# Kernel tuning notes

Hardware: AMD Instinct MI355X
Metric: run time of the kernel (lower is better)

The kernel has to match this reference:

```python
import jax, jax.numpy as jnp
import numpy as np

B, S, D, H = 8, 2048, 1024, 64

def setup_inputs() -> dict:
    key = jax.random.key(0)
    ks = jax.random.split(key, 7)
    scale = 0.02
    return {
        "x": jax.random.normal(ks[0], (B, S, D), dtype=jnp.float32),
        "Wq": jax.random.normal(ks[1], (D, H), dtype=jnp.float32) * scale,
        "bq": jax.random.normal(ks[2], (H,), dtype=jnp.float32) * scale,
        "Wk": jax.random.normal(ks[3], (D, H), dtype=jnp.float32) * scale,
        "bk": jax.random.normal(ks[4], (H,), dtype=jnp.float32) * scale,
        "Wv": jax.random.normal(ks[5], (D, H), dtype=jnp.float32) * scale,
        "bv": jax.random.normal(ks[6], (H,), dtype=jnp.float32) * scale,
    }

def reference(x, Wq, bq, Wk, bk, Wv, bv):
    # Single-head causal self-attention (dropout in eval mode -> identity).
    q = x @ Wq + bq            # [B,S,H]
    k = x @ Wk + bk            # [B,S,H]
    v = x @ Wv + bv            # [B,S,H]
    scores = jnp.einsum("bqh,bkh->bqk", q, k)  # [B,S,S]
    s = q.shape[1]
    causal = jnp.tril(jnp.ones((s, s), dtype=bool))
    # Original masks with -inf BEFORE scaling; -inf/scale == -inf, so equivalent.
    scores = jnp.where(causal, scores, -jnp.inf) / jnp.sqrt(jnp.float32(k.shape[-1]))
    attn = jax.nn.softmax(scores, axis=-1)
    return jnp.einsum("bqk,bkh->bqh", attn, v)
```

## Files before the change

kernel.cpp:

```cpp
#include <hip/hip_runtime.h>
#include <math.h>

#define BATCH 8
#define SEQ   2048
#define DIM   1024
#define HD    64
#define NROWS (BATCH * SEQ)
#define CHUNK 256
#define NCHUNK 8
#define QTILE 32
#define NQT   (SEQ / QTILE)

typedef __attribute__((ext_vector_type(8))) short bf16x8;
typedef __attribute__((ext_vector_type(4))) float f32x4;

__device__ __forceinline__ unsigned short f2bf(float f) {
    unsigned u = __float_as_uint(f);
    u = (u + 0x7FFFu + ((u >> 16) & 1u)) >> 16;
    return (unsigned short)u;
}

__device__ __forceinline__ void gld_lds16(const void* g, void* l) {
    __builtin_amdgcn_global_load_lds(
        (const __attribute__((address_space(1))) void*)g,
        (__attribute__((address_space(3))) void*)l, 16, 0, 0);
}


__global__ __launch_bounds__(256)
void prep_w_kernel(const float* __restrict__ Wq, const float* __restrict__ Wk,
                   const float* __restrict__ Wv, unsigned short* __restrict__ Wt)
{
    const int mat = blockIdx.y;
    const float* __restrict__ W = (mat == 0) ? Wq : (mat == 1) ? Wk : Wv;
    const int k0 = blockIdx.x * 64;
    __shared__ float T[64][65];
    const int t = threadIdx.x;
    #pragma unroll
    for (int i = 0; i < 16; ++i) {
        const int idx = t + i * 256;
        T[idx >> 6][idx & 63] = W[(size_t)(k0 + (idx >> 6)) * HD + (idx & 63)];
    }
    __syncthreads();
    const int n = t >> 2;
    const int c = t & 3;
    union { unsigned short h[16]; uint4 v[2]; } buf;
    #pragma unroll
    for (int j = 0; j < 16; ++j) buf.h[j] = f2bf(T[c * 16 + j][n]);
    unsigned short* dst = Wt + ((size_t)mat * HD + n) * DIM + k0 + c * 16;
    *(uint4*)dst       = buf.v[0];
    *(uint4*)(dst + 8) = buf.v[1];
}

__global__ __launch_bounds__(384)
void qkv_mfma_kernel(const float* __restrict__ x,
                     const unsigned short* __restrict__ Wt,
                     const float* __restrict__ bq, const float* __restrict__ bk,
                     const float* __restrict__ bv,
                     unsigned short* __restrict__ Qg,
                     unsigned short* __restrict__ Kg,
                     unsigned short* __restrict__ Vtg)
{
    __shared__ unsigned short Xs[32][64];
    __shared__ unsigned short Ws[192][64];

    const int t    = threadIdx.x;
    const int lane = t & 63;
    const int w    = t >> 6;
    const int col  = lane & 15;
    const int quad = lane >> 4;
    const int rh   = w & 1;
    const int mat  = w >> 1;
    const int row0 = blockIdx.x * 32;

    const int r8 = lane >> 3, ch = lane & 7;
    const int xr = t >> 3,  xc = t & 7;

    f32x4 acc[4];
    #pragma unroll
    for (int i = 0; i < 4; ++i) acc[i] = (f32x4){0.f, 0.f, 0.f, 0.f};

    const int swzr = (ch ^ r8) * 8;

    for (int k0 = 0; k0 < DIM; k0 += 64) {
        __syncthreads();
        #pragma unroll
        for (int ii = 0; ii < 4; ++ii) {
            const int rbase = w * 32 + ii * 8;
            gld_lds16(&Wt[(size_t)(rbase + r8) * DIM + k0 + swzr], &Ws[rbase][0]);
        }
        if (t < 256) {
            const float* xp = &x[(size_t)(row0 + xr) * DIM + k0 + xc * 8];
            const float4 v0 = *(const float4*)xp;
            const float4 v1 = *(const float4*)(xp + 4);
            uint4 o;
            o.x = (unsigned)f2bf(v0.x) | ((unsigned)f2bf(v0.y) << 16);
            o.y = (unsigned)f2bf(v0.z) | ((unsigned)f2bf(v0.w) << 16);
            o.z = (unsigned)f2bf(v1.x) | ((unsigned)f2bf(v1.y) << 16);
            o.w = (unsigned)f2bf(v1.z) | ((unsigned)f2bf(v1.w) << 16);
            *(uint4*)&Xs[xr][(xc ^ (xr & 7)) * 8] = o;
        }
        __syncthreads();
        #pragma unroll
        for (int ks = 0; ks < 2; ++ks) {
            const int fswz = ((ks * 4 + quad) ^ (col & 7)) * 8;
            const bf16x8 a = *(const bf16x8*)&Xs[rh * 16 + col][fswz];
            #pragma unroll
            for (int nt = 0; nt < 4; ++nt) {
                const bf16x8 b = *(const bf16x8*)&Ws[mat * 64 + nt * 16 + col][fswz];
                acc[nt] = __builtin_amdgcn_mfma_f32_16x16x32_bf16(a, b, acc[nt], 0, 0, 0);
            }
        }
    }

    const int b    = row0 / SEQ;
    const int s0   = (row0 % SEQ) + rh * 16 + quad * 4;
    const int grow = row0 + rh * 16 + quad * 4;
    const float* __restrict__ bias = (mat == 0) ? bq : (mat == 1) ? bk : bv;
    #pragma unroll
    for (int nt = 0; nt < 4; ++nt) {
        const int nn = nt * 16 + col;
        const float bvv = bias[nn];
        if (mat < 2) {
            unsigned short* __restrict__ o = (mat == 0) ? Qg : Kg;
            #pragma unroll
            for (int r = 0; r < 4; ++r)
                o[(size_t)(grow + r) * HD + nn] = f2bf(acc[nt][r] + bvv);
        } else {
            const unsigned lo = (unsigned)f2bf(acc[nt][0] + bvv) | ((unsigned)f2bf(acc[nt][1] + bvv) << 16);
            const unsigned hi = (unsigned)f2bf(acc[nt][2] + bvv) | ((unsigned)f2bf(acc[nt][3] + bvv) << 16);
            *(uint2*)&Vtg[((size_t)b * HD + nn) * SEQ + s0] = make_uint2(lo, hi);
        }
    }
}

__global__ __launch_bounds__(128)
void attn_part_kernel(const unsigned short* __restrict__ Qg,
                      const unsigned short* __restrict__ Kg,
                      const unsigned short* __restrict__ Vtg,
                      float* __restrict__ Opart,
                      float* __restrict__ ML)
{
    const int xb = blockIdx.x;
    const int c  = xb >> 9;
    const int b  = (xb >> 6) & 7;
    const int qt = xb & 63;
    if (qt < c * 8) return;

    __shared__ unsigned short Ks[64][64];
    __shared__ unsigned short Vs[64][64];
    __shared__ unsigned short Ps[2][16][72];

    const int t    = threadIdx.x;
    const int w    = t >> 6;
    const int lane = t & 63;
    const int col  = lane & 15;
    const int quad = lane >> 4;
    const int q0w  = qt * QTILE + w * 16;
    const size_t gq = (size_t)b * SEQ + q0w;

    const bf16x8 aq0 = *(const bf16x8*)&Qg[(gq + col) * HD + quad * 8];
    const bf16x8 aq1 = *(const bf16x8*)&Qg[(gq + col) * HD + 32 + quad * 8];

    f32x4 oacc[4];
    #pragma unroll
    for (int n = 0; n < 4; ++n) oacc[n] = (f32x4){0.f, 0.f, 0.f, 0.f};
    float mrow[4], lrow[4];
    #pragma unroll
    for (int r = 0; r < 4; ++r) { mrow[r] = -INFINITY; lrow[r] = 0.f; }

    const int kbeg   = c * CHUNK;
    const int kend   = min((c + 1) * CHUNK, (qt + 1) * QTILE);
    const int ntiles = (kend - kbeg + 63) >> 6;

    const int r8 = lane >> 3, ch = lane & 7;
    const int swzr = (ch ^ r8) * 8;
    const unsigned short* kgb = Kg  + (size_t)b * SEQ * HD;
    const unsigned short* vgb = Vtg + (size_t)b * HD * SEQ;

    for (int it = 0; it < ntiles; ++it) {
        const int j0 = kbeg + it * 64;
        __syncthreads();
        #pragma unroll
        for (int ii = 0; ii < 4; ++ii) {
            const int rb = w * 32 + ii * 8;
            gld_lds16(&kgb[(size_t)(j0 + rb + r8) * HD + swzr], &Ks[rb][0]);
            gld_lds16(&vgb[(size_t)(rb + r8) * SEQ + j0 + swzr], &Vs[rb][0]);
        }
        __syncthreads();

        if (j0 <= q0w + 15) {
            f32x4 scv[4];
            #pragma unroll
            for (int nt = 0; nt < 4; ++nt) {
                const int sw0 = (quad ^ (col & 7)) * 8;
                const int sw1 = ((4 + quad) ^ (col & 7)) * 8;
                const bf16x8 bk0 = *(const bf16x8*)&Ks[nt * 16 + col][sw0];
                const bf16x8 bk1 = *(const bf16x8*)&Ks[nt * 16 + col][sw1];
                f32x4 s = __builtin_amdgcn_mfma_f32_16x16x32_bf16(aq0, bk0, (f32x4){0.f,0.f,0.f,0.f}, 0, 0, 0);
                s = __builtin_amdgcn_mfma_f32_16x16x32_bf16(aq1, bk1, s, 0, 0, 0);
                scv[nt] = s;
            }
            const bool needmask = (j0 + 63 > q0w);
            #pragma unroll
            for (int r = 0; r < 4; ++r) {
                const int row = q0w + quad * 4 + r;
                float sv[4];
                float tmax = -INFINITY;
                if (needmask) {
                    #pragma unroll
                    for (int nt = 0; nt < 4; ++nt) {
                        const int key = j0 + nt * 16 + col;
                        sv[nt] = (key <= row) ? scv[nt][r] * 0.125f : -INFINITY;
                        tmax = fmaxf(tmax, sv[nt]);
                    }
                } else {
                    #pragma unroll
                    for (int nt = 0; nt < 4; ++nt) {
                        sv[nt] = scv[nt][r] * 0.125f;
                        tmax = fmaxf(tmax, sv[nt]);
                    }
                }
                #pragma unroll
                for (int off = 1; off < 16; off <<= 1)
                    tmax = fmaxf(tmax, __shfl_xor(tmax, off, 64));
                const float mnew  = fmaxf(mrow[r], tmax);
                const float alpha = __expf(mrow[r] - mnew);
                mrow[r] = mnew;
                float psum = 0.f;
                #pragma unroll
                for (int nt = 0; nt < 4; ++nt) {
                    const float p = __expf(sv[nt] - mnew);
                    psum += p;
                    Ps[w][quad * 4 + r][nt * 16 + col] = f2bf(p);
                }
                #pragma unroll
                for (int off = 1; off < 16; off <<= 1)
                    psum += __shfl_xor(psum, off, 64);
                lrow[r] = lrow[r] * alpha + psum;
                #pragma unroll
                for (int n = 0; n < 4; ++n) oacc[n][r] *= alpha;
            }
            #pragma unroll
            for (int ks = 0; ks < 2; ++ks) {
                const bf16x8 ap = *(const bf16x8*)&Ps[w][col][ks * 32 + quad * 8];
                const int fswz = ((ks * 4 + quad) ^ (col & 7)) * 8;
                #pragma unroll
                for (int n = 0; n < 4; ++n) {
                    const bf16x8 bv2 = *(const bf16x8*)&Vs[n * 16 + col][fswz];
                    oacc[n] = __builtin_amdgcn_mfma_f32_16x16x32_bf16(ap, bv2, oacc[n], 0, 0, 0);
                }
            }
        }
    }

    const int blk = (b * NQT + qt) * NCHUNK + c;
    float* Ob = Opart + (size_t)blk * (QTILE * HD);
    #pragma unroll
    for (int n = 0; n < 4; ++n)
        #pragma unroll
        for (int r = 0; r < 4; ++r)
            Ob[(w * 16 + quad * 4 + r) * HD + n * 16 + col] = oacc[n][r];
    if (col == 0) {
        float* mlb = ML + (size_t)blk * 64;
        #pragma unroll
        for (int r = 0; r < 4; ++r) {
            mlb[w * 16 + quad * 4 + r]      = mrow[r];
            mlb[32 + w * 16 + quad * 4 + r] = lrow[r];
        }
    }
}

__global__ __launch_bounds__(256)
void combine_kernel(const float* __restrict__ Opart,
                    const float* __restrict__ ML,
                    float* __restrict__ out)
{
    const int gid = blockIdx.x * 256 + threadIdx.x;
    const int i   = gid >> 6;
    const int d   = gid & 63;
    const int b   = i >> 11;
    const int s   = i & 2047;
    const int qt  = s >> 5;
    const int r32 = s & 31;
    const int nc  = (s >> 8) + 1;
    const int blk0 = (b * NQT + qt) * NCHUNK;

    float M = -INFINITY;
    for (int cc = 0; cc < nc; ++cc)
        M = fmaxf(M, ML[(size_t)(blk0 + cc) * 64 + r32]);
    float L = 0.f, acc = 0.f;
    for (int cc = 0; cc < nc; ++cc) {
        const float m = ML[(size_t)(blk0 + cc) * 64 + r32];
        const float l = ML[(size_t)(blk0 + cc) * 64 + 32 + r32];
        const float e = __expf(m - M);
        L   += l * e;
        acc += e * Opart[(size_t)(blk0 + cc) * (QTILE * HD) + r32 * HD + d];
    }
    out[(size_t)i * HD + d] = acc / L;
}

extern "C" void kernel_launch(void* const* d_in, const int* in_sizes, int n_in,
                              void* d_out, int out_size, void* d_ws, size_t ws_size,
                              hipStream_t stream) {
    const float* x  = (const float*)d_in[0];
    const float* Wq = (const float*)d_in[1];
    const float* bq = (const float*)d_in[2];
    const float* Wk = (const float*)d_in[3];
    const float* bk = (const float*)d_in[4];
    const float* Wv = (const float*)d_in[5];
    const float* bv = (const float*)d_in[6];
    float* out = (float*)d_out;

    unsigned short* Wt  = (unsigned short*)d_ws;
    unsigned short* Qg  = Wt + (size_t)3 * HD * DIM;
    unsigned short* Kg  = Qg + (size_t)NROWS * HD;
    unsigned short* Vtg = Kg + (size_t)NROWS * HD;
    float* Opart = (float*)(Vtg + (size_t)BATCH * HD * SEQ);
    float* ML    = Opart + (size_t)BATCH * NQT * NCHUNK * QTILE * HD;

    prep_w_kernel<<<dim3(16, 3), 256, 0, stream>>>(Wq, Wk, Wv, Wt);
    qkv_mfma_kernel<<<dim3(NROWS / 32), 384, 0, stream>>>(x, Wt, bq, bk, bv, Qg, Kg, Vtg);
    attn_part_kernel<<<dim3(NCHUNK * BATCH * NQT), 128, 0, stream>>>(Qg, Kg, Vtg, Opart, ML);
    combine_kernel<<<dim3(NROWS * HD / 256), 256, 0, stream>>>(Opart, ML, out);
}
```

Before: 160.1 us.

## Enlarge attention query tile to 64 and QKV K-step to 128

Measured after the change: 165.7 us. 3.5% more time.

```diff
diff --git a/kernel.cpp b/kernel.cpp
--- a/kernel.cpp
+++ b/kernel.cpp
@@ -8,7 +8,7 @@
 #define NROWS (BATCH * SEQ)
 #define CHUNK 256
 #define NCHUNK 8
-#define QTILE 32
+#define QTILE 64
 #define NQT   (SEQ / QTILE)
 
 typedef __attribute__((ext_vector_type(8))) short bf16x8;
@@ -61,8 +61,8 @@
                      unsigned short* __restrict__ Kg,
                      unsigned short* __restrict__ Vtg)
 {
-    __shared__ unsigned short Xs[32][64];
-    __shared__ unsigned short Ws[192][64];
+    __shared__ unsigned short Xs[32][128];
+    __shared__ unsigned short Ws[192][128];
 
     const int t    = threadIdx.x;
     const int lane = t & 63;
@@ -73,37 +73,42 @@
     const int mat  = w >> 1;
     const int row0 = blockIdx.x * 32;
 
-    const int r8 = lane >> 3, ch = lane & 7;
-    const int xr = t >> 3,  xc = t & 7;
+    const int r4   = lane >> 4;
+    const int ch16 = lane & 15;
 
     f32x4 acc[4];
     #pragma unroll
     for (int i = 0; i < 4; ++i) acc[i] = (f32x4){0.f, 0.f, 0.f, 0.f};
 
-    const int swzr = (ch ^ r8) * 8;
-
-    for (int k0 = 0; k0 < DIM; k0 += 64) {
+    for (int k0 = 0; k0 < DIM; k0 += 128) {
         __syncthreads();
         #pragma unroll
-        for (int ii = 0; ii < 4; ++ii) {
-            const int rbase = w * 32 + ii * 8;
-            gld_lds16(&Wt[(size_t)(rbase + r8) * DIM + k0 + swzr], &Ws[rbase][0]);
+        for (int ii = 0; ii < 8; ++ii) {
+            const int rbase = w * 32 + ii * 4;
+            const int r = rbase + r4;
+            gld_lds16(&Wt[(size_t)r * DIM + k0 + (ch16 ^ (r & 15)) * 8], &Ws[rbase][0]);
         }
         if (t < 256) {
-            const float* xp = &x[(size_t)(row0 + xr) * DIM + k0 + xc * 8];
-            const float4 v0 = *(const float4*)xp;
-            const float4 v1 = *(const float4*)(xp + 4);
-            uint4 o;
-            o.x = (unsigned)f2bf(v0.x) | ((unsigned)f2bf(v0.y) << 16);
-            o.y = (unsigned)f2bf(v0.z) | ((unsigned)f2bf(v0.w) << 16);
-            o.z = (unsigned)f2bf(v1.x) | ((unsigned)f2bf(v1.y) << 16);
-            o.w = (unsigned)f2bf(v1.z) | ((unsigned)f2bf(v1.w) << 16);
-            *(uint4*)&Xs[xr][(xc ^ (xr & 7)) * 8] = o;
+            const int xr  = t >> 3;
+            const int xc0 = t & 7;
+            #pragma unroll
+            for (int h = 0; h < 2; ++h) {
+                const int g = xc0 + h * 8;
+                const float* xp = &x[(size_t)(row0 + xr) * DIM + k0 + g * 8];
+                const float4 v0 = *(const float4*)xp;
+                const float4 v1 = *(const float4*)(xp + 4);
+                uint4 o;
+                o.x = (unsigned)f2bf(v0.x) | ((unsigned)f2bf(v0.y) << 16);
+                o.y = (unsigned)f2bf(v0.z) | ((unsigned)f2bf(v0.w) << 16);
+                o.z = (unsigned)f2bf(v1.x) | ((unsigned)f2bf(v1.y) << 16);
+                o.w = (unsigned)f2bf(v1.z) | ((unsigned)f2bf(v1.w) << 16);
+                *(uint4*)&Xs[xr][(g ^ (xr & 15)) * 8] = o;
+            }
         }
         __syncthreads();
         #pragma unroll
-        for (int ks = 0; ks < 2; ++ks) {
-            const int fswz = ((ks * 4 + quad) ^ (col & 7)) * 8;
+        for (int ks = 0; ks < 4; ++ks) {
+            const int fswz = ((ks * 4 + quad) ^ col) * 8;
             const bf16x8 a = *(const bf16x8*)&Xs[rh * 16 + col][fswz];
             #pragma unroll
             for (int nt = 0; nt < 4; ++nt) {
@@ -134,7 +139,7 @@
     }
 }
 
-__global__ __launch_bounds__(128)
+__global__ __launch_bounds__(256)
 void attn_part_kernel(const unsigned short* __restrict__ Qg,
                       const unsigned short* __restrict__ Kg,
                       const unsigned short* __restrict__ Vtg,
@@ -142,14 +147,14 @@
                       float* __restrict__ ML)
 {
     const int xb = blockIdx.x;
-    const int c  = xb >> 9;
-    const int b  = (xb >> 6) & 7;
-    const int qt = xb & 63;
-    if (qt < c * 8) return;
+    const int c  = xb >> 8;
+    const int b  = (xb >> 5) & 7;
+    const int qt = xb & 31;
+    if (qt < c * 4) return;
 
     __shared__ unsigned short Ks[64][64];
     __shared__ unsigned short Vs[64][64];
-    __shared__ unsigned short Ps[2][16][72];
+    __shared__ unsigned short Ps[4][16][76];
 
     const int t    = threadIdx.x;
     const int w    = t >> 6;
@@ -182,8 +187,8 @@
         const int j0 = kbeg + it * 64;
         __syncthreads();
         #pragma unroll
-        for (int ii = 0; ii < 4; ++ii) {
-            const int rb = w * 32 + ii * 8;
+        for (int ii = 0; ii < 2; ++ii) {
+            const int rb = w * 16 + ii * 8;
             gld_lds16(&kgb[(size_t)(j0 + rb + r8) * HD + swzr], &Ks[rb][0]);
             gld_lds16(&vgb[(size_t)(rb + r8) * SEQ + j0 + swzr], &Vs[rb][0]);
         }
@@ -262,11 +267,11 @@
         for (int r = 0; r < 4; ++r)
             Ob[(w * 16 + quad * 4 + r) * HD + n * 16 + col] = oacc[n][r];
     if (col == 0) {
-        float* mlb = ML + (size_t)blk * 64;
+        float* mlb = ML + (size_t)blk * 128;
         #pragma unroll
         for (int r = 0; r < 4; ++r) {
             mlb[w * 16 + quad * 4 + r]      = mrow[r];
-            mlb[32 + w * 16 + quad * 4 + r] = lrow[r];
+            mlb[64 + w * 16 + quad * 4 + r] = lrow[r];
         }
     }
 }
@@ -281,21 +286,21 @@
     const int d   = gid & 63;
     const int b   = i >> 11;
     const int s   = i & 2047;
-    const int qt  = s >> 5;
-    const int r32 = s & 31;
+    const int qt  = s >> 6;
+    const int r64 = s & 63;
     const int nc  = (s >> 8) + 1;
     const int blk0 = (b * NQT + qt) * NCHUNK;
 
     float M = -INFINITY;
     for (int cc = 0; cc < nc; ++cc)
-        M = fmaxf(M, ML[(size_t)(blk0 + cc) * 64 + r32]);
+        M = fmaxf(M, ML[(size_t)(blk0 + cc) * 128 + r64]);
     float L = 0.f, acc = 0.f;
     for (int cc = 0; cc < nc; ++cc) {
-        const float m = ML[(size_t)(blk0 + cc) * 64 + r32];
-        const float l = ML[(size_t)(blk0 + cc) * 64 + 32 + r32];
+        const float m = ML[(size_t)(blk0 + cc) * 128 + r64];
+        const float l = ML[(size_t)(blk0 + cc) * 128 + 64 + r64];
         const float e = __expf(m - M);
         L   += l * e;
-        acc += e * Opart[(size_t)(blk0 + cc) * (QTILE * HD) + r32 * HD + d];
+        acc += e * Opart[(size_t)(blk0 + cc) * (QTILE * HD) + r64 * HD + d];
     }
     out[(size_t)i * HD + d] = acc / L;
 }
@@ -321,6 +326,6 @@
 
     prep_w_kernel<<<dim3(16, 3), 256, 0, stream>>>(Wq, Wk, Wv, Wt);
     qkv_mfma_kernel<<<dim3(NROWS / 32), 384, 0, stream>>>(x, Wt, bq, bk, bv, Qg, Kg, Vtg);
-    attn_part_kernel<<<dim3(NCHUNK * BATCH * NQT), 128, 0, stream>>>(Qg, Kg, Vtg, Opart, ML);
+    attn_part_kernel<<<dim3(NCHUNK * BATCH * NQT), 256, 0, stream>>>(Qg, Kg, Vtg, Opart, ML);
     combine_kernel<<<dim3(NROWS * HD / 256), 256, 0, stream>>>(Opart, ML, out);
 }
```
